# Performance work log

Measured on AMD Instinct MI355X. Metric: run time of the kernel, lower is better.

## Reference

```python
import jax, jax.numpy as jnp
import numpy as np


def fwht(x):
    """Normalized fast Walsh-Hadamard transform over the last dim (power of 2).
    Equivalent to x @ H_n / sqrt(n) with H symmetric, so it serves as both
    matmul_hadU and matmul_hadUt in QuIP#."""
    n = x.shape[-1]
    steps = int(np.log2(n))
    assert 1 << steps == n
    shape = x.shape
    x = x.reshape(-1, n)
    h = 1
    for _ in range(steps):
        x = x.reshape(-1, n // (2 * h), 2, h)
        a = x[:, :, 0, :]
        b = x[:, :, 1, :]
        x = jnp.stack([a + b, a - b], axis=2).reshape(-1, n)
        h *= 2
    return (x * np.float32(1.0 / np.sqrt(n))).reshape(shape)


def setup_inputs() -> dict:
    key = jax.random.key(0)
    ks = jax.random.split(key, 9)
    B, S = 4, 2048
    n_in, n_out, codesz, cb_size, rank = 4096, 4096, 4, 256, 64
    inputs = {
        "input": jax.random.normal(ks[0], (B, S, n_in), dtype=jnp.float32),
        "Qidxs": jax.random.randint(ks[1], (n_out, n_in // codesz), 0, cb_size, dtype=jnp.int32),
        "D4_CB": jax.random.normal(ks[2], (cb_size, codesz), dtype=jnp.float32),
        # SU / SV are random sign (+-1) vectors from the randomized Hadamard transform
        "SU": jnp.where(jax.random.bernoulli(ks[3], 0.5, (n_in,)), 1.0, -1.0).astype(jnp.float32),
        "SV": jnp.where(jax.random.bernoulli(ks[4], 0.5, (n_out,)), 1.0, -1.0).astype(jnp.float32),
        "Wscale": jnp.float32(0.9),
        "A": jax.random.normal(ks[5], (n_out, rank), dtype=jnp.float32) * 0.02,
        "B": jax.random.normal(ks[6], (rank, n_in), dtype=jnp.float32) * 0.02,
        # positive per-input-channel rescale
        "scaleWH": jax.random.uniform(ks[7], (n_in,), dtype=jnp.float32, minval=0.5, maxval=1.5),
    }
    return inputs


def reference(input, Qidxs, D4_CB, SU, SV, Wscale, A, B, scaleWH):
    n_out, n_groups = Qidxs.shape
    codesz = D4_CB.shape[1]
    n_in = n_groups * codesz
    lead = input.shape[:-1]

    x = input.reshape(-1, n_in)            # [T, n_in]
    x = x / scaleWH                        # rescale_WH
    x = x * SU                             # input sign flips
    x = fwht(x)                            # matmul_hadUt
    Bx = x @ B.T                           # [T, rank] low-rank path

    # Dequantize: gather codebook vectors and flatten groups -> [n_out, n_in]
    W_hat = D4_CB[Qidxs].reshape(n_out, n_in)
    z = x @ W_hat.T                        # [T, n_out]

    z = z * Wscale
    z = z + Bx @ A.T                       # low-rank correction
    z = fwht(z)                            # matmul_hadU on output dim
    z = z * SV                             # output sign flips
    return z.reshape(*lead, n_out)
```

## Files before the change

### kernel.cpp

```cpp
#include <hip/hip_runtime.h>
#include <hip/hip_bf16.h>
#include <stdint.h>

typedef __attribute__((ext_vector_type(8))) short short8;
typedef __attribute__((ext_vector_type(4))) float floatx4;

#define GLOAD_LDS16(gptr, lptr)                                                     \
  __builtin_amdgcn_global_load_lds(                                                 \
      (const __attribute__((address_space(1))) void*)(gptr),                        \
      (__attribute__((address_space(3))) void*)(lptr), 16, 0, 0)

#define FENCE() asm volatile("" ::: "memory")
#define BARRIER() do { FENCE(); __builtin_amdgcn_s_barrier(); FENCE(); } while (0)
#define PHASE_END() do { __builtin_amdgcn_sched_barrier(0);                        \
                         asm volatile("s_waitcnt lgkmcnt(0)" ::: "memory");        \
                         __builtin_amdgcn_s_barrier();                             \
                         __builtin_amdgcn_sched_barrier(0); } while (0)

__device__ inline void fwht16(float v[16]) {
#pragma unroll
    for (int s = 0; s < 4; ++s) {
        const int h = 1 << s;
#pragma unroll
        for (int k = 0; k < 16; k += 2 * h)
#pragma unroll
            for (int j = 0; j < h; ++j) {
                float a = v[k + j], b = v[k + j + h];
                v[k + j] = a + b;
                v[k + j + h] = a - b;
            }
    }
}

__global__ __launch_bounds__(512) void decode_mfma(
    const int* __restrict__ Qidxs, const float* __restrict__ D4_CB,
    const float* __restrict__ Wscale_p, const float* __restrict__ A,
    const float* __restrict__ B, __hip_bfloat16* __restrict__ W_eff)
{
    __shared__ __align__(16) __hip_bfloat16 la[256 * 72];
    __shared__ __align__(16) __hip_bfloat16 lbt[256 * 72];
    __shared__ __align__(16) float CBs[1024];

    const int t = threadIdx.x;
    const int lane = t & 63;
    const int wv = t >> 6;
    const int wm = wv >> 2;
    const int wn = wv & 3;
    const long oBase = (long)blockIdx.y * 256;
    const long iBase = (long)blockIdx.x * 256;

#pragma unroll
    for (int u = 0; u < 8; ++u) {
        int el4 = u * 512 + t;
        int row = el4 >> 4;
        int r   = (el4 & 15) * 4;
        float4 v = *(const float4*)(A + (oBase + row) * 64 + r);
        __hip_bfloat16* d = &la[row * 72 + r];
        d[0] = __float2bfloat16(v.x); d[1] = __float2bfloat16(v.y);
        d[2] = __float2bfloat16(v.z); d[3] = __float2bfloat16(v.w);
    }
#pragma unroll
    for (int u = 0; u < 32; ++u) {
        int el = u * 512 + t;
        int r = el >> 8;
        int j = el & 255;
        lbt[j * 72 + r] = __float2bfloat16(B[(long)r * 4096 + iBase + j]);
    }
    if (t < 256) ((float4*)CBs)[t] = ((const float4*)D4_CB)[t];
    __syncthreads();

    const float wscale = Wscale_p[0];
    const int fr = lane & 15;
    const int c2 = lane >> 4;
    floatx4 acc[8][4] = {};
    short8 af[4][2], bfx[4][2];

#pragma unroll
    for (int n = 0; n < 4; ++n)
#pragma unroll
        for (int kh = 0; kh < 2; ++kh)
            bfx[n][kh] = *(const short8*)&lbt[(wn * 64 + n * 16 + fr) * 72 + kh * 32 + c2 * 8];

#pragma unroll
    for (int mh = 0; mh < 2; ++mh) {
#pragma unroll
        for (int m = 0; m < 4; ++m)
#pragma unroll
            for (int kh = 0; kh < 2; ++kh)
                af[m][kh] = *(const short8*)&la[(wm * 128 + mh * 64 + m * 16 + fr) * 72 + kh * 32 + c2 * 8];
#pragma unroll
        for (int m = 0; m < 4; ++m)
#pragma unroll
            for (int n = 0; n < 4; ++n)
#pragma unroll
                for (int kh = 0; kh < 2; ++kh)
                    acc[mh * 4 + m][n] = __builtin_amdgcn_mfma_f32_16x16x32_bf16(
                        af[m][kh], bfx[n][kh], acc[mh * 4 + m][n], 0, 0, 0);
    }

    const int q4 = c2 * 4;
#pragma unroll
    for (int m = 0; m < 8; ++m)
#pragma unroll
        for (int n = 0; n < 4; ++n)
#pragma unroll
            for (int rr = 0; rr < 4; ++rr) {
                const long o = oBase + wm * 128 + m * 16 + q4 + rr;
                const long i = iBase + wn * 64 + n * 16 + fr;
                const int q = Qidxs[o * 1024 + (i >> 2)];
                const float w = wscale * CBs[q * 4 + (i & 3)] + acc[m][n][rr];
                W_eff[o * 4096 + i] = __float2bfloat16(w);
            }
}

__global__ __launch_bounds__(256) void fwht_in_kernel(
    const float* __restrict__ x, const float* __restrict__ SU,
    const float* __restrict__ sWH, __hip_bfloat16* __restrict__ xh)
{
    __shared__ float row[4096 + 256];
    const int t = threadIdx.x;
    const long base = (long)blockIdx.x * 4096;
    float v[16];

#pragma unroll
    for (int u = 0; u < 16; ++u) {
        int e = u * 256 + t;
        v[u] = x[base + e] / sWH[e] * SU[e];
    }
    fwht16(v);
#pragma unroll
    for (int u = 0; u < 16; ++u) {
        int e = u * 256 + t;
        row[e + (e >> 4)] = v[u];
    }
    __syncthreads();

    const int lo = t & 15, hi = t >> 4;
#pragma unroll
    for (int u = 0; u < 16; ++u) v[u] = row[hi * 272 + u * 17 + lo];
    fwht16(v);
#pragma unroll
    for (int u = 0; u < 16; ++u) row[hi * 272 + u * 17 + lo] = v[u];
    __syncthreads();

#pragma unroll
    for (int u = 0; u < 16; ++u) v[u] = row[t * 17 + u];
    fwht16(v);

    short8 o0, o1;
#pragma unroll
    for (int u = 0; u < 8; ++u) {
        __hip_bfloat16 b = __float2bfloat16(v[u] * 0.015625f);
        o0[u] = *(short*)&b;
    }
#pragma unroll
    for (int u = 0; u < 8; ++u) {
        __hip_bfloat16 b = __float2bfloat16(v[8 + u] * 0.015625f);
        o1[u] = *(short*)&b;
    }
    *(short8*)(xh + base + t * 16) = o0;
    *(short8*)(xh + base + t * 16 + 8) = o1;
}

__global__ __launch_bounds__(512, 2) void gemm_bt(
    const __hip_bfloat16* __restrict__ xh,
    const __hip_bfloat16* __restrict__ wf,
    __hip_bfloat16* __restrict__ z)
{
    __shared__ __align__(16) __hip_bfloat16 sA[2][256 * 64];
    __shared__ __align__(16) __hip_bfloat16 sB[2][256 * 64];

    const int t = threadIdx.x;
    const int lane = t & 63;
    const int wv = t >> 6;
    const int wm = wv >> 2;
    const int wn = wv & 3;
    const long mBase = (long)blockIdx.y * 256;
    const long nBase = (long)blockIdx.x * 256;

    const int grow = t >> 3;
    const int gcol = ((t & 7) ^ (grow & 7)) * 8;
    const __hip_bfloat16* gA = xh + (mBase + grow) * 4096 + gcol;
    const __hip_bfloat16* gB = wf + (nBase + grow) * 4096 + gcol;
    const int lrow = wv * 8;

    const int fr = lane & 15;
    const int c2 = lane >> 4;
    const int slot0 = ((c2 ^ (fr & 7)) * 8);

    floatx4 acc[8][4] = {};
    short8 afr[4][2];
    short8 bfr[4][2];

    auto stage = [&](int buf, int isA, int halfRow, int kt) {
        const __hip_bfloat16* g =
            (isA ? gA : gB) + (long)halfRow * 4096 + (long)kt * 64;
        __hip_bfloat16* l =
            (isA ? &sA[buf][0] : &sB[buf][0]) + (halfRow + lrow) * 64;
        GLOAD_LDS16(g, l);
        GLOAD_LDS16(g + 64L * 4096, l + 64 * 64);
    };
    auto ldA = [&](int buf, int mhalf) {
        const __hip_bfloat16* base =
            &sA[buf][0] + (wm * 128 + mhalf * 64 + fr) * 64;
#pragma unroll
        for (int m = 0; m < 4; ++m) {
            afr[m][0] = *(const short8*)(base + m * 16 * 64 + slot0);
            afr[m][1] = *(const short8*)(base + m * 16 * 64 + (slot0 ^ 32));
        }
    };
    auto ldB2 = [&](int buf, int npair) {
        const __hip_bfloat16* base =
            &sB[buf][0] + (wn * 64 + npair * 32 + fr) * 64;
#pragma unroll
        for (int n = 0; n < 2; ++n) {
            bfr[npair * 2 + n][0] = *(const short8*)(base + n * 16 * 64 + slot0);
            bfr[npair * 2 + n][1] = *(const short8*)(base + n * 16 * 64 + (slot0 ^ 32));
        }
    };
    auto mma16 = [&](int mh, int np) {
#pragma unroll
        for (int m = 0; m < 4; ++m)
#pragma unroll
            for (int n = 0; n < 2; ++n)
#pragma unroll
                for (int kh = 0; kh < 2; ++kh)
                    acc[mh * 4 + m][np * 2 + n] =
                        __builtin_amdgcn_mfma_f32_16x16x32_bf16(
                            afr[m][kh], bfr[np * 2 + n][kh],
                            acc[mh * 4 + m][np * 2 + n], 0, 0, 0);
    };

    stage(0, 1, 0,   0);
    stage(0, 1, 128, 0);
    stage(0, 0, 0,   0);
    stage(0, 0, 128, 0);
    stage(1, 0, 0,   1);
    stage(1, 1, 0,   1);
    asm volatile("s_waitcnt vmcnt(4)" ::: "memory");
    BARRIER();

    for (int kt = 0; kt < 64; ++kt) {
        const int cur = kt & 1;

        ldA(cur, 0);
        ldB2(cur, 0);
        if (kt + 1 < 64) stage(cur ^ 1, 1, 128, kt + 1);
        __builtin_amdgcn_s_setprio(1);
        mma16(0, 0);
        __builtin_amdgcn_s_setprio(0);
        PHASE_END();

        ldB2(cur, 1);
        if (kt + 1 < 64) stage(cur ^ 1, 0, 128, kt + 1);
        __builtin_amdgcn_s_setprio(1);
        mma16(0, 1);
        __builtin_amdgcn_s_setprio(0);
        PHASE_END();

        ldA(cur, 1);
        if (kt + 2 < 64) stage(cur, 0, 0, kt + 2);
        __builtin_amdgcn_s_setprio(1);
        mma16(1, 0);
        __builtin_amdgcn_s_setprio(0);
        PHASE_END();

        if (kt + 2 < 64) stage(cur, 1, 0, kt + 2);
        __builtin_amdgcn_s_setprio(1);
        mma16(1, 1);
        __builtin_amdgcn_s_setprio(0);
        __builtin_amdgcn_sched_barrier(0);
        if (kt < 62) asm volatile("s_waitcnt vmcnt(4) lgkmcnt(0)" ::: "memory");
        else         asm volatile("s_waitcnt vmcnt(0) lgkmcnt(0)" ::: "memory");
        __builtin_amdgcn_s_barrier();
        __builtin_amdgcn_sched_barrier(0);
    }

    const int q4 = c2 * 4;
#pragma unroll
    for (int m = 0; m < 8; ++m)
#pragma unroll
        for (int n = 0; n < 4; ++n)
#pragma unroll
            for (int r = 0; r < 4; ++r) {
                const long row = mBase + wm * 128 + m * 16 + q4 + r;
                const long col = nBase + wn * 64 + n * 16 + fr;
                z[row * 4096 + col] = __float2bfloat16(acc[m][n][r]);
            }
}

__global__ __launch_bounds__(256) void fwht_out_kernel(
    const __hip_bfloat16* __restrict__ z, const float* __restrict__ SV,
    float* __restrict__ out)
{
    __shared__ float row[4096 + 256];
    const int t = threadIdx.x;
    const long base = (long)blockIdx.x * 4096;
    float v[16];

#pragma unroll
    for (int u = 0; u < 16; ++u) {
        int e = u * 256 + t;
        v[u] = __bfloat162float(z[base + e]);
    }
    fwht16(v);
#pragma unroll
    for (int u = 0; u < 16; ++u) {
        int e = u * 256 + t;
        row[e + (e >> 4)] = v[u];
    }
    __syncthreads();

    const int lo = t & 15, hi = t >> 4;
#pragma unroll
    for (int u = 0; u < 16; ++u) v[u] = row[hi * 272 + u * 17 + lo];
    fwht16(v);
#pragma unroll
    for (int u = 0; u < 16; ++u) row[hi * 272 + u * 17 + lo] = v[u];
    __syncthreads();

#pragma unroll
    for (int u = 0; u < 16; ++u) v[u] = row[t * 17 + u];
    fwht16(v);

    const float4* svv = (const float4*)(SV + t * 16);
    float4* ov = (float4*)(out + base + t * 16);
#pragma unroll
    for (int c = 0; c < 4; ++c) {
        float4 s = svv[c];
        float4 f;
        f.x = v[4 * c + 0] * s.x * 0.015625f;
        f.y = v[4 * c + 1] * s.y * 0.015625f;
        f.z = v[4 * c + 2] * s.z * 0.015625f;
        f.w = v[4 * c + 3] * s.w * 0.015625f;
        ov[c] = f;
    }
}

extern "C" void kernel_launch(void* const* d_in, const int* in_sizes, int n_in,
                              void* d_out, int out_size, void* d_ws, size_t ws_size,
                              hipStream_t stream)
{
    const float* input  = (const float*)d_in[0];
    const int*   Qidxs  = (const int*)d_in[1];
    const float* D4_CB  = (const float*)d_in[2];
    const float* SU     = (const float*)d_in[3];
    const float* SV     = (const float*)d_in[4];
    const float* Wscale = (const float*)d_in[5];
    const float* A      = (const float*)d_in[6];
    const float* B      = (const float*)d_in[7];
    const float* sWH    = (const float*)d_in[8];
    float* out = (float*)d_out;

    char* ws = (char*)d_ws;
    __hip_bfloat16* weff = (__hip_bfloat16*)ws;
    __hip_bfloat16* xh   = (__hip_bfloat16*)(ws + (32L << 20));
    __hip_bfloat16* zbuf = (__hip_bfloat16*)(ws + (32L << 20) + (64L << 20));

    decode_mfma<<<dim3(16, 16), 512, 0, stream>>>(Qidxs, D4_CB, Wscale, A, B, weff);
    fwht_in_kernel<<<8192, 256, 0, stream>>>(input, SU, sWH, xh);
    gemm_bt<<<dim3(16, 32), 512, 0, stream>>>(xh, weff, zbuf);
    fwht_out_kernel<<<8192, 256, 0, stream>>>(zbuf, SV, out);
}
```

Before: 552.1 us.

## Fold output Hadamard and SV sign flips into the effective weight matrix

Applies the output-dimension FWHT and SV scaling to the dequantized weight matrix (in fp32, via three column passes) instead of to the activations. The GEMM now writes fp32 output directly, which removes the bf16 z buffer and the separate output FWHT kernel. It also swaps the divide by scaleWH for a reciprocal multiply. The cost is extra per-call passes over a 4096x4096 fp32 weight temp (64MB read and write per pass) and a slightly different rounding order.

```diff
diff --git a/kernel.cpp b/kernel.cpp
--- a/kernel.cpp
+++ b/kernel.cpp
@@ -3,6 +3,7 @@
 #include <stdint.h>
 
 typedef __attribute__((ext_vector_type(8))) short short8;
+typedef __attribute__((ext_vector_type(4))) short short4v;
 typedef __attribute__((ext_vector_type(4))) float floatx4;
 
 #define GLOAD_LDS16(gptr, lptr)                                                     \
@@ -32,10 +33,25 @@
     }
 }
 
+__device__ inline void fwht16v(floatx4 v[16]) {
+#pragma unroll
+    for (int s = 0; s < 4; ++s) {
+        const int h = 1 << s;
+#pragma unroll
+        for (int k = 0; k < 16; k += 2 * h)
+#pragma unroll
+            for (int j = 0; j < h; ++j) {
+                floatx4 a = v[k + j], b = v[k + j + h];
+                v[k + j] = a + b;
+                v[k + j + h] = a - b;
+            }
+    }
+}
+
 __global__ __launch_bounds__(512) void decode_mfma(
     const int* __restrict__ Qidxs, const float* __restrict__ D4_CB,
     const float* __restrict__ Wscale_p, const float* __restrict__ A,
-    const float* __restrict__ B, __hip_bfloat16* __restrict__ W_eff)
+    const float* __restrict__ B, float* __restrict__ W_tmp)
 {
     __shared__ __align__(16) __hip_bfloat16 la[256 * 72];
     __shared__ __align__(16) __hip_bfloat16 lbt[256 * 72];
@@ -108,9 +124,44 @@
                 const long o = oBase + wm * 128 + m * 16 + q4 + rr;
                 const long i = iBase + wn * 64 + n * 16 + fr;
                 const int q = Qidxs[o * 1024 + (i >> 2)];
-                const float w = wscale * CBs[q * 4 + (i & 3)] + acc[m][n][rr];
-                W_eff[o * 4096 + i] = __float2bfloat16(w);
-            }
+                W_tmp[o * 4096 + i] = wscale * CBs[q * 4 + (i & 3)] + acc[m][n][rr];
+            }
+}
+
+__global__ __launch_bounds__(256) void wfwht_col_pass(
+    const float* __restrict__ Win, float* __restrict__ Wf,
+    __hip_bfloat16* __restrict__ Wb, const float* __restrict__ SV,
+    int s4, int last)
+{
+    const int g = blockIdx.x;
+    const int col = blockIdx.y * 1024 + threadIdx.x * 4;
+    const int st = 1 << s4;
+    const int base_o = ((g >> s4) << (s4 + 4)) | (g & (st - 1));
+
+    floatx4 v[16];
+#pragma unroll
+    for (int j = 0; j < 16; ++j)
+        v[j] = *(const floatx4*)(Win + (long)(base_o + j * st) * 4096 + col);
+    fwht16v(v);
+
+    if (!last) {
+#pragma unroll
+        for (int j = 0; j < 16; ++j)
+            *(floatx4*)(Wf + (long)(base_o + j * st) * 4096 + col) = v[j];
+    } else {
+#pragma unroll
+        for (int j = 0; j < 16; ++j) {
+            const long o = base_o + (long)j * st;
+            const float sc = SV[o] * 0.015625f;
+            short4v p;
+#pragma unroll
+            for (int c = 0; c < 4; ++c) {
+                __hip_bfloat16 b = __float2bfloat16(v[j][c] * sc);
+                p[c] = *(short*)&b;
+            }
+            *(short4v*)(Wb + o * 4096 + col) = p;
+        }
+    }
 }
 
 __global__ __launch_bounds__(256) void fwht_in_kernel(
@@ -125,7 +176,7 @@
 #pragma unroll
     for (int u = 0; u < 16; ++u) {
         int e = u * 256 + t;
-        v[u] = x[base + e] / sWH[e] * SU[e];
+        v[u] = x[base + e] * (SU[e] * __builtin_amdgcn_rcpf(sWH[e]));
     }
     fwht16(v);
 #pragma unroll
@@ -165,7 +216,7 @@
 __global__ __launch_bounds__(512, 2) void gemm_bt(
     const __hip_bfloat16* __restrict__ xh,
     const __hip_bfloat16* __restrict__ wf,
-    __hip_bfloat16* __restrict__ z)
+    float* __restrict__ out)
 {
     __shared__ __align__(16) __hip_bfloat16 sA[2][256 * 64];
     __shared__ __align__(16) __hip_bfloat16 sB[2][256 * 64];
@@ -285,56 +336,8 @@
             for (int r = 0; r < 4; ++r) {
                 const long row = mBase + wm * 128 + m * 16 + q4 + r;
                 const long col = nBase + wn * 64 + n * 16 + fr;
-                z[row * 4096 + col] = __float2bfloat16(acc[m][n][r]);
-            }
-}
-
-__global__ __launch_bounds__(256) void fwht_out_kernel(
-    const __hip_bfloat16* __restrict__ z, const float* __restrict__ SV,
-    float* __restrict__ out)
-{
-    __shared__ float row[4096 + 256];
-    const int t = threadIdx.x;
-    const long base = (long)blockIdx.x * 4096;
-    float v[16];
-
-#pragma unroll
-    for (int u = 0; u < 16; ++u) {
-        int e = u * 256 + t;
-        v[u] = __bfloat162float(z[base + e]);
-    }
-    fwht16(v);
-#pragma unroll
-    for (int u = 0; u < 16; ++u) {
-        int e = u * 256 + t;
-        row[e + (e >> 4)] = v[u];
-    }
-    __syncthreads();
-
-    const int lo = t & 15, hi = t >> 4;
-#pragma unroll
-    for (int u = 0; u < 16; ++u) v[u] = row[hi * 272 + u * 17 + lo];
-    fwht16(v);
-#pragma unroll
-    for (int u = 0; u < 16; ++u) row[hi * 272 + u * 17 + lo] = v[u];
-    __syncthreads();
-
-#pragma unroll
-    for (int u = 0; u < 16; ++u) v[u] = row[t * 17 + u];
-    fwht16(v);
-
-    const float4* svv = (const float4*)(SV + t * 16);
-    float4* ov = (float4*)(out + base + t * 16);
-#pragma unroll
-    for (int c = 0; c < 4; ++c) {
-        float4 s = svv[c];
-        float4 f;
-        f.x = v[4 * c + 0] * s.x * 0.015625f;
-        f.y = v[4 * c + 1] * s.y * 0.015625f;
-        f.z = v[4 * c + 2] * s.z * 0.015625f;
-        f.w = v[4 * c + 3] * s.w * 0.015625f;
-        ov[c] = f;
-    }
+                out[row * 4096 + col] = acc[m][n][r];
+            }
 }
 
 extern "C" void kernel_launch(void* const* d_in, const int* in_sizes, int n_in,
@@ -353,12 +356,14 @@
     float* out = (float*)d_out;
 
     char* ws = (char*)d_ws;
-    __hip_bfloat16* weff = (__hip_bfloat16*)ws;
+    __hip_bfloat16* w4   = (__hip_bfloat16*)ws;
     __hip_bfloat16* xh   = (__hip_bfloat16*)(ws + (32L << 20));
-    __hip_bfloat16* zbuf = (__hip_bfloat16*)(ws + (32L << 20) + (64L << 20));
-
-    decode_mfma<<<dim3(16, 16), 512, 0, stream>>>(Qidxs, D4_CB, Wscale, A, B, weff);
+    float*          wtmp = (float*)(ws + (32L << 20) + (64L << 20));
+
+    decode_mfma<<<dim3(16, 16), 512, 0, stream>>>(Qidxs, D4_CB, Wscale, A, B, wtmp);
+    wfwht_col_pass<<<dim3(256, 4), 256, 0, stream>>>(wtmp, wtmp, nullptr, nullptr, 0, 0);
+    wfwht_col_pass<<<dim3(256, 4), 256, 0, stream>>>(wtmp, wtmp, nullptr, nullptr, 4, 0);
+    wfwht_col_pass<<<dim3(256, 4), 256, 0, stream>>>(wtmp, nullptr, w4, SV, 8, 1);
     fwht_in_kernel<<<8192, 256, 0, stream>>>(input, SU, sWH, xh);
-    gemm_bt<<<dim3(16, 32), 512, 0, stream>>>(xh, weff, zbuf);
-    fwht_out_kernel<<<8192, 256, 0, stream>>>(zbuf, SV, out);
-}
+    gemm_bt<<<dim3(16, 32), 512, 0, stream>>>(xh, w4, out);
+}
```

After: 591.7 us. 7.2% more time.
